# Optimization experiments

Measured on AMD Instinct MI355X. Metric: run time of the kernel, lower is better.

Reference implementation:

```python
import jax
import jax.numpy as jnp
import numpy as np
from jax import lax

B, S, C, H, O = 32, 128, 128, 128, 64  # batch, rows(seq), cols, hidden, output classes


def setup_inputs() -> dict:
    key = jax.random.key(0)
    ks = jax.random.split(key, 12)
    s = 1.0 / np.sqrt(H)  # PyTorch GRU/Linear default init scale
    u = lambda k, shape: jax.random.uniform(k, shape, jnp.float32, -s, s)
    return {
        "x": jax.random.normal(ks[0], (B, S, C), jnp.float32),
        "h_prev": jnp.zeros((2, B, H), jnp.float32),  # [fwd; bwd] initial hidden
        "Wih_f": u(ks[1], (3 * H, 1)),
        "Whh_f": u(ks[2], (3 * H, H)),
        "bih_f": u(ks[3], (3 * H,)),
        "bhh_f": u(ks[4], (3 * H,)),
        "Wih_b": u(ks[5], (3 * H, 1)),
        "Whh_b": u(ks[6], (3 * H, H)),
        "bih_b": u(ks[7], (3 * H,)),
        "bhh_b": u(ks[8], (3 * H,)),
        "W_fc": u(ks[9], (O, 2 * H)),
        "b_fc": u(ks[10], (O,)),
    }


def _gru_cell(h, xt, Wih, Whh, bih, bhh):
    # xt: (B, 1), h: (B, H). PyTorch gate order: r, z, n.
    gi = xt @ Wih.T + bih            # (B, 3H)
    gh = h @ Whh.T + bhh             # (B, 3H)
    ir, iz, inn = jnp.split(gi, 3, axis=-1)
    hr, hz, hn = jnp.split(gh, 3, axis=-1)
    r = jax.nn.sigmoid(ir + hr)
    z = jax.nn.sigmoid(iz + hz)
    n = jnp.tanh(inn + r * hn)
    return (1.0 - z) * n + z * h


def reference(x, h_prev, Wih_f, Whh_f, bih_f, bhh_f, Wih_b, Whh_b, bih_b, bhh_b, W_fc, b_fc):
    # x: (B, S, C). Loop over columns; each column (B, S) is a length-S scalar
    # sequence fed to a bidirectional GRU; final hidden state chains to the next column.

    def step(hs, xs):
        hf, hb = hs
        xf, xb = xs  # each (B,)
        hf = _gru_cell(hf, xf[:, None], Wih_f, Whh_f, bih_f, bhh_f)
        hb = _gru_cell(hb, xb[:, None], Wih_b, Whh_b, bih_b, bhh_b)
        return (hf, hb), None

    step = jax.checkpoint(step)

    def column(carry, col):  # col: (B, S)
        col_rev = col[:, ::-1]
        (hf, hb), _ = lax.scan(step, carry, (col.T, col_rev.T))  # scan over S
        # torch: cat(out[:, -1, :H], out[:, 0, H:]) == (fwd final hidden, bwd final hidden)
        feat = jnp.concatenate([hf, hb], axis=-1)                 # (B, 2H)
        out = jax.nn.softmax(jax.nn.relu(feat @ W_fc.T + b_fc), axis=-1)  # (B, O)
        return (hf, hb), out

    cols = jnp.moveaxis(x, 2, 0)  # (C, B, S)
    _, outs = lax.scan(column, (h_prev[0], h_prev[1]), cols)  # outs: (C, B, O)
    return jnp.transpose(outs, (1, 0, 2))  # (B, C, O)
```

## Files before the change

### kernel.cpp

```cpp
#include <hip/hip_runtime.h>
#include <hip/hip_bf16.h>

#define BB 32
#define SS 128
#define CC 128
#define HH 128
#define OO 64

typedef _Float16 f16;
typedef f16 h2 __attribute__((ext_vector_type(2)));
typedef unsigned u32x4 __attribute__((ext_vector_type(4)));

__device__ __forceinline__ float exp2n(float x) {
    float r; asm("v_exp_f32 %0, %1" : "=v"(r) : "v"(x)); return r;
}
__device__ __forceinline__ float rcpn(float x) {
    float r; asm("v_rcp_f32 %0, %1" : "=v"(r) : "v"(x)); return r;
}

__device__ __forceinline__ float dpp_add_x1(float v) {
    int m = __builtin_amdgcn_update_dpp(0, __builtin_bit_cast(int, v),
                                        0xB1, 0xF, 0xF, true);
    return v + __builtin_bit_cast(float, m);
}

__device__ __forceinline__ h2 as_h2(unsigned u) { return __builtin_bit_cast(h2, u); }

__device__ __forceinline__ unsigned pack2f(float a, float b) {
    h2 v; v[0] = (f16)a; v[1] = (f16)b;
    return __builtin_bit_cast(unsigned, v);
}
__device__ __forceinline__ u32x4 packrow8(const float* p) {
    u32x4 r;
    r.x = pack2f(p[0], p[1]);
    r.y = pack2f(p[2], p[3]);
    r.z = pack2f(p[4], p[5]);
    r.w = pack2f(p[6], p[7]);
    return r;
}

__device__ __forceinline__ float dot4x2(u32x4 w, u32x4 h, float acc) {
    acc = __builtin_amdgcn_fdot2(as_h2(w.x), as_h2(h.x), acc, false);
    acc = __builtin_amdgcn_fdot2(as_h2(w.y), as_h2(h.y), acc, false);
    acc = __builtin_amdgcn_fdot2(as_h2(w.z), as_h2(h.z), acc, false);
    acc = __builtin_amdgcn_fdot2(as_h2(w.w), as_h2(h.w), acc, false);
    return acc;
}

__global__
__attribute__((amdgpu_flat_work_group_size(256, 256), amdgpu_waves_per_eu(1, 2)))
void gru_chain_kernel(
    const float* __restrict__ x,
    const float* __restrict__ h_prev,
    const float* __restrict__ Wih_f, const float* __restrict__ Whh_f,
    const float* __restrict__ bih_f, const float* __restrict__ bhh_f,
    const float* __restrict__ Wih_b, const float* __restrict__ Whh_b,
    const float* __restrict__ bih_b, const float* __restrict__ bhh_b,
    float* __restrict__ hsnap)
{
    const int wg   = blockIdx.x;
    const int d    = wg >> 5;
    const int b    = wg & 31;
    const int t    = threadIdx.x;
    const int j    = t >> 1;
    const int half = t & 1;

    const float* __restrict__ Wih = d ? Wih_b : Wih_f;
    const float* __restrict__ Whh = d ? Whh_b : Whh_f;
    const float* __restrict__ bih = d ? bih_b : bih_f;
    const float* __restrict__ bhh = d ? bhh_b : bhh_f;

    __shared__ float xs[SS * CC + 4608];
    __shared__ __align__(16) f16 hbuf[2][160];

    {
        const float4* xb4 = reinterpret_cast<const float4*>(x + (size_t)b * SS * CC);
        float4* xs4 = reinterpret_cast<float4*>(xs);
        #pragma unroll
        for (int i = 0; i < 16; ++i) xs4[t + i * 256] = xb4[t + i * 256];
    }

    const float* rowr = Whh + (j          ) * HH + half * 64;
    const float* rowz = Whh + (j +     HH ) * HH + half * 64;
    const float* rown = Whh + (j + 2 * HH ) * HH + half * 64;
    u32x4 wr0 = packrow8(rowr +  0), wr1 = packrow8(rowr +  8),
          wr2 = packrow8(rowr + 16), wr3 = packrow8(rowr + 24),
          wr4 = packrow8(rowr + 32), wr5 = packrow8(rowr + 40),
          wr6 = packrow8(rowr + 48), wr7 = packrow8(rowr + 56);
    u32x4 wz0 = packrow8(rowz +  0), wz1 = packrow8(rowz +  8),
          wz2 = packrow8(rowz + 16), wz3 = packrow8(rowz + 24),
          wz4 = packrow8(rowz + 32), wz5 = packrow8(rowz + 40),
          wz6 = packrow8(rowz + 48), wz7 = packrow8(rowz + 56);
    u32x4 wn0 = packrow8(rown +  0), wn1 = packrow8(rown +  8),
          wn2 = packrow8(rown + 16), wn3 = packrow8(rown + 24),
          wn4 = packrow8(rown + 32), wn5 = packrow8(rown + 40),
          wn6 = packrow8(rown + 48), wn7 = packrow8(rown + 56);
    asm volatile("" : "+v"(wr0), "+v"(wr1), "+v"(wr2), "+v"(wr3),
                      "+v"(wr4), "+v"(wr5), "+v"(wr6), "+v"(wr7),
                      "+v"(wz0), "+v"(wz1), "+v"(wz2), "+v"(wz3));
    asm volatile("" : "+v"(wz4), "+v"(wz5), "+v"(wz6), "+v"(wz7),
                      "+v"(wn0), "+v"(wn1), "+v"(wn2), "+v"(wn3),
                      "+v"(wn4), "+v"(wn5), "+v"(wn6), "+v"(wn7));

    const float L1 = 1.44269504f;
    const float wihr_s = -L1 * Wih[j];
    const float wihz_s = -L1 * Wih[j + HH];
    const float wihn_s = 2.0f * L1 * Wih[j + 2 * HH];
    const float bihn_s = 2.0f * L1 * bih[j + 2 * HH];
    const float brz_r2 = 0.5f * (bih[j]      + bhh[j]);
    const float brz_z2 = 0.5f * (bih[j + HH] + bhh[j + HH]);
    const float bhh_n2 = 0.5f * bhh[j + 2 * HH];

    float hp = h_prev[(d * BB + b) * HH + j];
    const int hwr = ((j >> 6) * 72) + (j & 63);
    if (half == 0) hbuf[0][hwr] = (f16)hp;
    __syncthreads();

#define GSTEP(SRC, DST, TSS)                                                   \
    {                                                                          \
        const int tt = d ? (SS - 1 - (TSS)) : (TSS);                           \
        const float xv = xs[tt * CC + c];          \
        const u32x4* hb =                                                      \
            reinterpret_cast<const u32x4*>(&hbuf[SRC][half * 72]);             \
        const u32x4 h0 = hb[0], h1 = hb[1], h2 = hb[2], h3 = hb[3],            \
                    h4 = hb[4], h5 = hb[5], h6 = hb[6], h7 = hb[7];            \
        float r0 = dot4x2(wr0, h0, brz_r2), r1 = dot4x2(wr1, h1, 0.f),         \
              r2 = dot4x2(wr2, h2, 0.f),    r3 = dot4x2(wr3, h3, 0.f);         \
        float z0 = dot4x2(wz0, h0, brz_z2), z1 = dot4x2(wz1, h1, 0.f),         \
              z2 = dot4x2(wz2, h2, 0.f),    z3 = dot4x2(wz3, h3, 0.f);         \
        float n0 = dot4x2(wn0, h0, bhh_n2), n1 = dot4x2(wn1, h1, 0.f),         \
              n2 = dot4x2(wn2, h2, 0.f),    n3 = dot4x2(wn3, h3, 0.f);         \
        r0 = dot4x2(wr4, h4, r0); r1 = dot4x2(wr5, h5, r1);                    \
        r2 = dot4x2(wr6, h6, r2); r3 = dot4x2(wr7, h7, r3);                    \
        z0 = dot4x2(wz4, h4, z0); z1 = dot4x2(wz5, h5, z1);                    \
        z2 = dot4x2(wz6, h6, z2); z3 = dot4x2(wz7, h7, z3);                    \
        n0 = dot4x2(wn4, h4, n0); n1 = dot4x2(wn5, h5, n1);                    \
        n2 = dot4x2(wn6, h6, n2); n3 = dot4x2(wn7, h7, n3);                    \
        float sr = (r0 + r1) + (r2 + r3);                                      \
        float sz = (z0 + z1) + (z2 + z3);                                      \
        float sn = (n0 + n1) + (n2 + n3);                                      \
        sr = dpp_add_x1(sr);                             \
        sz = dpp_add_x1(sz);                                                   \
        sn = dpp_add_x1(sn);                                                   \
                                   \
        const float argr = fmaf(sr, -L1, xv * wihr_s);                         \
        const float argz = fmaf(sz, -L1, xv * wihz_s);                         \
        const float r = rcpn(1.0f + exp2n(argr));                              \
        const float z = rcpn(1.0f + exp2n(argz));                              \
        const float gin = fmaf(xv, wihn_s, bihn_s);                            \
        const float argn = fmaf(r, sn * (2.0f * L1), gin);                     \
        const float n = fmaf(-2.0f, rcpn(1.0f + exp2n(argn)), 1.0f);           \
        hp = fmaf(z, hp - n, n);                     \
        if (half == 0) hbuf[DST][hwr] = (f16)hp;                               \
        __syncthreads();                                                       \
    }

    for (int c = 0; c < CC; ++c) {
        for (int ts = 0; ts < SS; ts += 2) {
            GSTEP(0, 1, ts)
            GSTEP(1, 0, ts + 1)
        }
        if (half == 0) {
            hsnap[(((size_t)d * CC + c) * BB + b) * HH + j] = hp;
        }
    }
#undef GSTEP
}

__global__ __launch_bounds__(64) void fc_softmax_kernel(
    const float* __restrict__ hsnap,
    const float* __restrict__ W_fc,
    const float* __restrict__ b_fc,
    float* __restrict__ out)
{
    const int cb = blockIdx.x;
    const int c  = cb >> 5;
    const int b  = cb & 31;
    const int o  = threadIdx.x;

    __shared__ float feat[2 * HH];
    #pragma unroll
    for (int i = 0; i < 4; ++i) {
        const int idx = i * 64 + o;
        const int dd  = idx >> 7;
        const int jj  = idx & (HH - 1);
        feat[idx] = hsnap[(((size_t)dd * CC + c) * BB + b) * HH + jj];
    }
    __syncthreads();

    float acc = 0.f;
    const float4* wrow = reinterpret_cast<const float4*>(W_fc + o * 2 * HH);
    const float4* f4   = reinterpret_cast<const float4*>(feat);
    #pragma unroll
    for (int k = 0; k < 64; ++k) {
        const float4 wv = wrow[k];
        const float4 fv = f4[k];
        acc = fmaf(wv.x, fv.x, acc);
        acc = fmaf(wv.y, fv.y, acc);
        acc = fmaf(wv.z, fv.z, acc);
        acc = fmaf(wv.w, fv.w, acc);
    }
    float v = fmaxf(acc + b_fc[o], 0.0f);

    float m = v;
    #pragma unroll
    for (int off = 32; off; off >>= 1) m = fmaxf(m, __shfl_xor(m, off));
    const float e = __expf(v - m);
    float ssum = e;
    #pragma unroll
    for (int off = 32; off; off >>= 1) ssum += __shfl_xor(ssum, off);

    out[((size_t)b * CC + c) * OO + o] = e / ssum;
}

extern "C" void kernel_launch(void* const* d_in, const int* in_sizes, int n_in,
                              void* d_out, int out_size, void* d_ws, size_t ws_size,
                              hipStream_t stream) {
    const float* x      = (const float*)d_in[0];
    const float* h_prev = (const float*)d_in[1];
    const float* Wih_f  = (const float*)d_in[2];
    const float* Whh_f  = (const float*)d_in[3];
    const float* bih_f  = (const float*)d_in[4];
    const float* bhh_f  = (const float*)d_in[5];
    const float* Wih_b  = (const float*)d_in[6];
    const float* Whh_b  = (const float*)d_in[7];
    const float* bih_b  = (const float*)d_in[8];
    const float* bhh_b  = (const float*)d_in[9];
    const float* W_fc   = (const float*)d_in[10];
    const float* b_fc   = (const float*)d_in[11];
    float* out   = (float*)d_out;
    float* hsnap = (float*)d_ws;

    gru_chain_kernel<<<64, 256, 0, stream>>>(x, h_prev, Wih_f, Whh_f, bih_f, bhh_f,
                                             Wih_b, Whh_b, bih_b, bhh_b, hsnap);
    fc_softmax_kernel<<<CC * BB, 64, 0, stream>>>(hsnap, W_fc, b_fc, out);
}
```

Before: 6.205 ms.

## Use one thread per hidden unit instead of two-lane split with DPP reduce

Changes the GRU recurrence kernel from 256 threads (two lanes per hidden unit, each holding half the weight row and combined via a DPP add) to 128 threads, each holding the full 128-wide row for r, z and n in registers. This removes the cross-lane DPP reduction and halves the number of waves that meet at each per-step barrier. In exchange, each thread does twice the dot-product work per step, reads the whole hidden vector from LDS and keeps about twice as many weight registers live, which lengthens the serial critical path per step.

After: 15.04 ms. 142% more time.

```diff
diff --git a/kernel.cpp b/kernel.cpp
--- a/kernel.cpp
+++ b/kernel.cpp
@@ -16,12 +16,6 @@
 }
 __device__ __forceinline__ float rcpn(float x) {
     float r; asm("v_rcp_f32 %0, %1" : "=v"(r) : "v"(x)); return r;
-}
-
-__device__ __forceinline__ float dpp_add_x1(float v) {
-    int m = __builtin_amdgcn_update_dpp(0, __builtin_bit_cast(int, v),
-                                        0xB1, 0xF, 0xF, true);
-    return v + __builtin_bit_cast(float, m);
 }
 
 __device__ __forceinline__ h2 as_h2(unsigned u) { return __builtin_bit_cast(h2, u); }
@@ -48,7 +42,7 @@
 }
 
 __global__
-__attribute__((amdgpu_flat_work_group_size(256, 256), amdgpu_waves_per_eu(1, 2)))
+__attribute__((amdgpu_flat_work_group_size(128, 128), amdgpu_waves_per_eu(1, 2)))
 void gru_chain_kernel(
     const float* __restrict__ x,
     const float* __restrict__ h_prev,
@@ -58,12 +52,11 @@
     const float* __restrict__ bih_b, const float* __restrict__ bhh_b,
     float* __restrict__ hsnap)
 {
-    const int wg   = blockIdx.x;
-    const int d    = wg >> 5;
-    const int b    = wg & 31;
-    const int t    = threadIdx.x;
-    const int j    = t >> 1;
-    const int half = t & 1;
+    const int wg = blockIdx.x;
+    const int d  = wg >> 5;
+    const int b  = wg & 31;
+    const int t  = threadIdx.x;
+    const int j  = t;
 
     const float* __restrict__ Wih = d ? Wih_b : Wih_f;
     const float* __restrict__ Whh = d ? Whh_b : Whh_f;
@@ -71,78 +64,104 @@
     const float* __restrict__ bhh = d ? bhh_b : bhh_f;
 
     __shared__ float xs[SS * CC + 4608];
-    __shared__ __align__(16) f16 hbuf[2][160];
+    __shared__ __align__(16) f16 hbuf[2][136];
 
     {
         const float4* xb4 = reinterpret_cast<const float4*>(x + (size_t)b * SS * CC);
         float4* xs4 = reinterpret_cast<float4*>(xs);
         #pragma unroll
-        for (int i = 0; i < 16; ++i) xs4[t + i * 256] = xb4[t + i * 256];
-    }
-
-    const float* rowr = Whh + (j          ) * HH + half * 64;
-    const float* rowz = Whh + (j +     HH ) * HH + half * 64;
-    const float* rown = Whh + (j + 2 * HH ) * HH + half * 64;
-    u32x4 wr0 = packrow8(rowr +  0), wr1 = packrow8(rowr +  8),
-          wr2 = packrow8(rowr + 16), wr3 = packrow8(rowr + 24),
-          wr4 = packrow8(rowr + 32), wr5 = packrow8(rowr + 40),
-          wr6 = packrow8(rowr + 48), wr7 = packrow8(rowr + 56);
-    u32x4 wz0 = packrow8(rowz +  0), wz1 = packrow8(rowz +  8),
-          wz2 = packrow8(rowz + 16), wz3 = packrow8(rowz + 24),
-          wz4 = packrow8(rowz + 32), wz5 = packrow8(rowz + 40),
-          wz6 = packrow8(rowz + 48), wz7 = packrow8(rowz + 56);
-    u32x4 wn0 = packrow8(rown +  0), wn1 = packrow8(rown +  8),
-          wn2 = packrow8(rown + 16), wn3 = packrow8(rown + 24),
-          wn4 = packrow8(rown + 32), wn5 = packrow8(rown + 40),
-          wn6 = packrow8(rown + 48), wn7 = packrow8(rown + 56);
+        for (int i = 0; i < 32; ++i) xs4[t + i * 128] = xb4[t + i * 128];
+    }
+
+    const float* rowr = Whh + (j          ) * HH;
+    const float* rowz = Whh + (j +     HH ) * HH;
+    const float* rown = Whh + (j + 2 * HH ) * HH;
+    u32x4 wr0 = packrow8(rowr +   0), wr1 = packrow8(rowr +   8),
+          wr2 = packrow8(rowr +  16), wr3 = packrow8(rowr +  24),
+          wr4 = packrow8(rowr +  32), wr5 = packrow8(rowr +  40),
+          wr6 = packrow8(rowr +  48), wr7 = packrow8(rowr +  56),
+          wr8 = packrow8(rowr +  64), wr9 = packrow8(rowr +  72),
+          wrA = packrow8(rowr +  80), wrB = packrow8(rowr +  88),
+          wrC = packrow8(rowr +  96), wrD = packrow8(rowr + 104),
+          wrE = packrow8(rowr + 112), wrF = packrow8(rowr + 120);
+    u32x4 wz0 = packrow8(rowz +   0), wz1 = packrow8(rowz +   8),
+          wz2 = packrow8(rowz +  16), wz3 = packrow8(rowz +  24),
+          wz4 = packrow8(rowz +  32), wz5 = packrow8(rowz +  40),
+          wz6 = packrow8(rowz +  48), wz7 = packrow8(rowz +  56),
+          wz8 = packrow8(rowz +  64), wz9 = packrow8(rowz +  72),
+          wzA = packrow8(rowz +  80), wzB = packrow8(rowz +  88),
+          wzC = packrow8(rowz +  96), wzD = packrow8(rowz + 104),
+          wzE = packrow8(rowz + 112), wzF = packrow8(rowz + 120);
+    u32x4 wn0 = packrow8(rown +   0), wn1 = packrow8(rown +   8),
+          wn2 = packrow8(rown +  16), wn3 = packrow8(rown +  24),
+          wn4 = packrow8(rown +  32), wn5 = packrow8(rown +  40),
+          wn6 = packrow8(rown +  48), wn7 = packrow8(rown +  56),
+          wn8 = packrow8(rown +  64), wn9 = packrow8(rown +  72),
+          wnA = packrow8(rown +  80), wnB = packrow8(rown +  88),
+          wnC = packrow8(rown +  96), wnD = packrow8(rown + 104),
+          wnE = packrow8(rown + 112), wnF = packrow8(rown + 120);
     asm volatile("" : "+v"(wr0), "+v"(wr1), "+v"(wr2), "+v"(wr3),
                       "+v"(wr4), "+v"(wr5), "+v"(wr6), "+v"(wr7),
-                      "+v"(wz0), "+v"(wz1), "+v"(wz2), "+v"(wz3));
-    asm volatile("" : "+v"(wz4), "+v"(wz5), "+v"(wz6), "+v"(wz7),
-                      "+v"(wn0), "+v"(wn1), "+v"(wn2), "+v"(wn3),
-                      "+v"(wn4), "+v"(wn5), "+v"(wn6), "+v"(wn7));
+                      "+v"(wr8), "+v"(wr9), "+v"(wrA), "+v"(wrB));
+    asm volatile("" : "+v"(wrC), "+v"(wrD), "+v"(wrE), "+v"(wrF),
+                      "+v"(wz0), "+v"(wz1), "+v"(wz2), "+v"(wz3),
+                      "+v"(wz4), "+v"(wz5), "+v"(wz6), "+v"(wz7));
+    asm volatile("" : "+v"(wz8), "+v"(wz9), "+v"(wzA), "+v"(wzB),
+                      "+v"(wzC), "+v"(wzD), "+v"(wzE), "+v"(wzF),
+                      "+v"(wn0), "+v"(wn1), "+v"(wn2), "+v"(wn3));
+    asm volatile("" : "+v"(wn4), "+v"(wn5), "+v"(wn6), "+v"(wn7),
+                      "+v"(wn8), "+v"(wn9), "+v"(wnA), "+v"(wnB),
+                      "+v"(wnC), "+v"(wnD), "+v"(wnE), "+v"(wnF));
 
     const float L1 = 1.44269504f;
     const float wihr_s = -L1 * Wih[j];
     const float wihz_s = -L1 * Wih[j + HH];
     const float wihn_s = 2.0f * L1 * Wih[j + 2 * HH];
     const float bihn_s = 2.0f * L1 * bih[j + 2 * HH];
-    const float brz_r2 = 0.5f * (bih[j]      + bhh[j]);
-    const float brz_z2 = 0.5f * (bih[j + HH] + bhh[j + HH]);
-    const float bhh_n2 = 0.5f * bhh[j + 2 * HH];
+    const float brz_r = bih[j]      + bhh[j];
+    const float brz_z = bih[j + HH] + bhh[j + HH];
+    const float bhh_n = bhh[j + 2 * HH];
 
     float hp = h_prev[(d * BB + b) * HH + j];
-    const int hwr = ((j >> 6) * 72) + (j & 63);
-    if (half == 0) hbuf[0][hwr] = (f16)hp;
+    hbuf[0][j] = (f16)hp;
     __syncthreads();
 
 #define GSTEP(SRC, DST, TSS)                                                   \
     {                                                                          \
         const int tt = d ? (SS - 1 - (TSS)) : (TSS);                           \
         const float xv = xs[tt * CC + c];          \
-        const u32x4* hb =                                                      \
-            reinterpret_cast<const u32x4*>(&hbuf[SRC][half * 72]);             \
-        const u32x4 h0 = hb[0], h1 = hb[1], h2 = hb[2], h3 = hb[3],            \
-                    h4 = hb[4], h5 = hb[5], h6 = hb[6], h7 = hb[7];            \
-        float r0 = dot4x2(wr0, h0, brz_r2), r1 = dot4x2(wr1, h1, 0.f),         \
-              r2 = dot4x2(wr2, h2, 0.f),    r3 = dot4x2(wr3, h3, 0.f);         \
-        float z0 = dot4x2(wz0, h0, brz_z2), z1 = dot4x2(wz1, h1, 0.f),         \
-              z2 = dot4x2(wz2, h2, 0.f),    z3 = dot4x2(wz3, h3, 0.f);         \
-        float n0 = dot4x2(wn0, h0, bhh_n2), n1 = dot4x2(wn1, h1, 0.f),         \
-              n2 = dot4x2(wn2, h2, 0.f),    n3 = dot4x2(wn3, h3, 0.f);         \
+        const u32x4* hb = reinterpret_cast<const u32x4*>(&hbuf[SRC][0]);       \
+        const u32x4 h0 = hb[0],  h1 = hb[1],  h2 = hb[2],  h3 = hb[3],         \
+                    h4 = hb[4],  h5 = hb[5],  h6 = hb[6],  h7 = hb[7],         \
+                    h8 = hb[8],  h9 = hb[9],  hA = hb[10], hB = hb[11],        \
+                    hC = hb[12], hD = hb[13], hE = hb[14], hF = hb[15];        \
+        float r0 = dot4x2(wr0, h0, brz_r), r1 = dot4x2(wr1, h1, 0.f),          \
+              r2 = dot4x2(wr2, h2, 0.f),   r3 = dot4x2(wr3, h3, 0.f);          \
+        float z0 = dot4x2(wz0, h0, brz_z), z1 = dot4x2(wz1, h1, 0.f),          \
+              z2 = dot4x2(wz2, h2, 0.f),   z3 = dot4x2(wz3, h3, 0.f);          \
+        float n0 = dot4x2(wn0, h0, bhh_n), n1 = dot4x2(wn1, h1, 0.f),          \
+              n2 = dot4x2(wn2, h2, 0.f),   n3 = dot4x2(wn3, h3, 0.f);          \
         r0 = dot4x2(wr4, h4, r0); r1 = dot4x2(wr5, h5, r1);                    \
         r2 = dot4x2(wr6, h6, r2); r3 = dot4x2(wr7, h7, r3);                    \
         z0 = dot4x2(wz4, h4, z0); z1 = dot4x2(wz5, h5, z1);                    \
         z2 = dot4x2(wz6, h6, z2); z3 = dot4x2(wz7, h7, z3);                    \
         n0 = dot4x2(wn4, h4, n0); n1 = dot4x2(wn5, h5, n1);                    \
         n2 = dot4x2(wn6, h6, n2); n3 = dot4x2(wn7, h7, n3);                    \
-        float sr = (r0 + r1) + (r2 + r3);                                      \
-        float sz = (z0 + z1) + (z2 + z3);                                      \
-        float sn = (n0 + n1) + (n2 + n3);                                      \
-        sr = dpp_add_x1(sr);                             \
-        sz = dpp_add_x1(sz);                                                   \
-        sn = dpp_add_x1(sn);                                                   \
-                                   \
+        r0 = dot4x2(wr8, h8, r0); r1 = dot4x2(wr9, h9, r1);                    \
+        r2 = dot4x2(wrA, hA, r2); r3 = dot4x2(wrB, hB, r3);                    \
+        z0 = dot4x2(wz8, h8, z0); z1 = dot4x2(wz9, h9, z1);                    \
+        z2 = dot4x2(wzA, hA, z2); z3 = dot4x2(wzB, hB, z3);                    \
+        n0 = dot4x2(wn8, h8, n0); n1 = dot4x2(wn9, h9, n1);                    \
+        n2 = dot4x2(wnA, hA, n2); n3 = dot4x2(wnB, hB, n3);                    \
+        r0 = dot4x2(wrC, hC, r0); r1 = dot4x2(wrD, hD, r1);                    \
+        r2 = dot4x2(wrE, hE, r2); r3 = dot4x2(wrF, hF, r3);                    \
+        z0 = dot4x2(wzC, hC, z0); z1 = dot4x2(wzD, hD, z1);                    \
+        z2 = dot4x2(wzE, hE, z2); z3 = dot4x2(wzF, hF, z3);                    \
+        n0 = dot4x2(wnC, hC, n0); n1 = dot4x2(wnD, hD, n1);                    \
+        n2 = dot4x2(wnE, hE, n2); n3 = dot4x2(wnF, hF, n3);                    \
+        const float sr = (r0 + r1) + (r2 + r3);                                \
+        const float sz = (z0 + z1) + (z2 + z3);                                \
+        const float sn = (n0 + n1) + (n2 + n3);                                \
         const float argr = fmaf(sr, -L1, xv * wihr_s);                         \
         const float argz = fmaf(sz, -L1, xv * wihz_s);                         \
         const float r = rcpn(1.0f + exp2n(argr));                              \
@@ -151,7 +170,7 @@
         const float argn = fmaf(r, sn * (2.0f * L1), gin);                     \
         const float n = fmaf(-2.0f, rcpn(1.0f + exp2n(argn)), 1.0f);           \
         hp = fmaf(z, hp - n, n);                     \
-        if (half == 0) hbuf[DST][hwr] = (f16)hp;                               \
+        hbuf[DST][j] = (f16)hp;                                                \
         __syncthreads();                                                       \
     }
 
@@ -160,9 +179,7 @@
             GSTEP(0, 1, ts)
             GSTEP(1, 0, ts + 1)
         }
-        if (half == 0) {
-            hsnap[(((size_t)d * CC + c) * BB + b) * HH + j] = hp;
-        }
+        hsnap[(((size_t)d * CC + c) * BB + b) * HH + j] = hp;
     }
 #undef GSTEP
 }
@@ -231,7 +248,7 @@
     float* out   = (float*)d_out;
     float* hsnap = (float*)d_ws;
 
-    gru_chain_kernel<<<64, 256, 0, stream>>>(x, h_prev, Wih_f, Whh_f, bih_f, bhh_f,
+    gru_chain_kernel<<<64, 128, 0, stream>>>(x, h_prev, Wih_f, Whh_f, bih_f, bhh_f,
                                              Wih_b, Whh_b, bih_b, bhh_b, hsnap);
     fc_softmax_kernel<<<CC * BB, 64, 0, stream>>>(hsnap, W_fc, b_fc, out);
 }
```
